# Kernel optimization log

Hardware: AMD Instinct MI355X
Metric: run time of the kernel (lower is better)

Reference implementation:

```python
import jax, jax.numpy as jnp
import numpy as np

N, E, D, H, C, ED = 50000, 800000, 128, 4, 32, 1
EFF = H * C  # 128 == D, so residual proj is Identity
FFN_H = 2 * EFF


def setup_inputs() -> dict:
    key = jax.random.key(0)
    ks = jax.random.split(key, 16)
    def p(k, shape, fan_in):
        return jax.random.normal(k, shape, dtype=jnp.float32) / np.sqrt(fan_in)
    return {
        "x": jax.random.normal(ks[0], (N, D), dtype=jnp.float32),
        "edge_attr": jax.random.normal(ks[1], (E, ED), dtype=jnp.float32),
        "W_l": p(ks[2], (D, EFF), D),
        "b_l": jnp.zeros((EFF,), jnp.float32),
        "W_r": p(ks[3], (D, EFF), D),
        "b_r": jnp.zeros((EFF,), jnp.float32),
        "W_e": p(ks[4], (ED, EFF), ED),
        "att": p(ks[5], (H, C), C),
        "bias_out": jnp.zeros((EFF,), jnp.float32),
        "W_gate": p(ks[6], (EFF, 1), EFF),
        "b_gate": jnp.zeros((1,), jnp.float32),
        "W_ffn1": p(ks[7], (EFF, FFN_H), EFF),
        "b_ffn1": jnp.zeros((FFN_H,), jnp.float32),
        "W_ffn2": p(ks[8], (FFN_H, EFF), FFN_H),
        "b_ffn2": jnp.zeros((EFF,), jnp.float32),
        "ln_gamma": jnp.ones((EFF,), jnp.float32),
        "ln_beta": jnp.zeros((EFF,), jnp.float32),
        "edge_index": jax.random.randint(ks[9], (2, E), 0, N, dtype=jnp.int32),
    }


def _gat_block(x, edge_attr, W_l, b_l, W_r, b_r, W_e, att, bias_out,
               W_gate, b_gate, W_ffn1, b_ffn1, W_ffn2, b_ffn2,
               ln_gamma, ln_beta, edge_index):
    n = x.shape[0]
    # add self loops (PyG default), edge_attr filled with mean
    loop = jnp.arange(n, dtype=edge_index.dtype)
    src = jnp.concatenate([edge_index[0], loop])
    dst = jnp.concatenate([edge_index[1], loop])
    ea = jnp.concatenate([edge_attr,
                          jnp.broadcast_to(edge_attr.mean(0, keepdims=True), (n, edge_attr.shape[1]))])
    # GATv2: separate source/target transforms + edge embedding
    xl = (x @ W_l + b_l).reshape(n, H, C)   # source features
    xr = (x @ W_r + b_r).reshape(n, H, C)   # target features
    ee = (ea @ W_e).reshape(-1, H, C)
    xj = xl[src]                             # [Et,H,C]
    m = jax.nn.leaky_relu(xj + xr[dst] + ee, negative_slope=0.2)
    logits = jnp.einsum('ehc,hc->eh', m, att)           # [Et,H]
    # segment softmax over destination nodes
    mx = jax.ops.segment_max(logits, dst, num_segments=n)
    ex = jnp.exp(logits - mx[dst])
    den = jax.ops.segment_sum(ex, dst, num_segments=n)
    alpha = ex / den[dst]
    out = jax.ops.segment_sum(xj * alpha[..., None], dst, num_segments=n)
    out = out.reshape(n, EFF) + bias_out
    # block: ELU, gated residual (proj is Identity since D==EFF), FFN, LayerNorm
    h = jax.nn.elu(out)
    gate = jax.nn.sigmoid(h @ W_gate + b_gate)
    y = gate * h + (1.0 - gate) * x
    ffn = jax.nn.relu(y @ W_ffn1 + b_ffn1) @ W_ffn2 + b_ffn2
    y = y + ffn
    mu = y.mean(-1, keepdims=True)
    var = y.var(-1, keepdims=True)
    y = (y - mu) * jax.lax.rsqrt(var + 1e-5) * ln_gamma + ln_beta
    return y  # dropout is identity in eval mode


def reference(x, edge_attr, W_l, b_l, W_r, b_r, W_e, att, bias_out,
              W_gate, b_gate, W_ffn1, b_ffn1, W_ffn2, b_ffn2,
              ln_gamma, ln_beta, edge_index):
    return _gat_block(x, edge_attr, W_l, b_l, W_r, b_r, W_e, att, bias_out,
                      W_gate, b_gate, W_ffn1, b_ffn1, W_ffn2, b_ffn2,
                      ln_gamma, ln_beta, edge_index)
```

## Files before the change

kernel.cpp:

```cpp
#include <hip/hip_runtime.h>
#include <hip/hip_bf16.h>

#define NODES 50000
#define NEDGE 800000
#define ETOT  850000

#define NRANGE 49
#define SB 256
#define ES ((ETOT + SB - 1) / SB)

#define XF_TILES 1563
#define HIST_BLKS 256
#define FUSE_GRID (2 * HIST_BLKS + (XF_TILES - HIST_BLKS))

typedef __hip_bfloat16 bf16;
typedef __attribute__((ext_vector_type(8))) short bf16x8;
typedef __attribute__((ext_vector_type(4))) float f32x4;

__device__ __forceinline__ bf16 f2bf(float v) { return __float2bfloat16(v); }
__device__ __forceinline__ float bflo(unsigned int v) { return __uint_as_float(v << 16); }
__device__ __forceinline__ float bfhi(unsigned int v) { return __uint_as_float(v & 0xffff0000u); }

__device__ __forceinline__ unsigned int pack2(float a, float b) {
    bf16 x = f2bf(a), y = f2bf(b);
    unsigned short xs = *reinterpret_cast<unsigned short*>(&x);
    unsigned short ys = *reinterpret_cast<unsigned short*>(&y);
    return ((unsigned int)ys << 16) | (unsigned int)xs;
}

__device__ __forceinline__ unsigned short bfbits(float v) {
    bf16 x = f2bf(v);
    return *reinterpret_cast<unsigned short*>(&x);
}

__device__ __forceinline__ void hilo(float v, unsigned short& h, unsigned short& l) {
    h = bfbits(v);
    float hv = __uint_as_float((unsigned int)h << 16);
    l = bfbits(v - hv);
}

__device__ __forceinline__ void split8(const float* v, bf16x8& hi, bf16x8& lo) {
    #pragma unroll
    for (int e = 0; e < 8; ++e) {
        unsigned short hb, lb;
        hilo(v[e], hb, lb);
        ((short*)&hi)[e] = (short)hb;
        ((short*)&lo)[e] = (short)lb;
    }
}

__global__ __launch_bounds__(256) void k_wx(const float* W_l, const float* W_r,
                                            const float* W1, const float* W2,
                                            bf16* wlh, bf16* wll,
                                            bf16* wrh, bf16* wrl,
                                            bf16* w1h, bf16* w1l,
                                            bf16* w2h, bf16* w2l) {
    int tid = blockIdx.x * blockDim.x + threadIdx.x;
    unsigned short h, l;
    if (tid < 32768) {
        int m = tid >> 14, t = tid & 16383;
        int c = t >> 7, k = t & 127;
        hilo((m ? W_r : W_l)[k * 128 + c], h, l);
        (m ? wrh : wlh)[t] = *(bf16*)&h;
        (m ? wrl : wll)[t] = *(bf16*)&l;
    } else if (tid < 65536) {
        int t = tid - 32768;
        int c = t >> 7, k = t & 127;
        hilo(W1[k * 256 + c], h, l);
        w1h[t] = *(bf16*)&h;
        w1l[t] = *(bf16*)&l;
    } else {
        int t = tid - 65536;
        int c = t >> 8, k = t & 255;
        hilo(W2[k * 128 + c], h, l);
        w2h[t] = *(bf16*)&h;
        w2l[t] = *(bf16*)&l;
    }
}

__global__ __launch_bounds__(256) void k_fuse(const float* edge_attr, const int* ei,
                                              float* sum_ea, int* rhist,
                                              const float* x,
                                              const bf16* wlh, const bf16* wll,
                                              const bf16* wrh, const bf16* wrl,
                                              const float* b_l, const float* b_r,
                                              bf16* xl, bf16* xr) {
    __shared__ __align__(16) float s_x[32][132];
    const int bid = blockIdx.x;
    int idx;
    bool isprep;
    if (bid < 2 * HIST_BLKS) { isprep = (bid & 1); idx = bid >> 1; }
    else { isprep = false; idx = HIST_BLKS + (bid - 2 * HIST_BLKS); }

    if (isprep) {
        int* hcnt = (int*)&s_x[0][0];
        const int t = threadIdx.x;
        if (t < 64) hcnt[t] = 0;
        __syncthreads();
        const int e0 = idx * ES;
        int e1 = e0 + ES; if (e1 > ETOT) e1 = ETOT;
        float local = 0.f;
        for (int e = e0 + t; e < e1; e += 256) {
            int dst = (e < NEDGE) ? ei[NEDGE + e] : (e - NEDGE);
            atomicAdd(&hcnt[dst >> 10], 1);
            if (e < NEDGE) local += edge_attr[e];
        }
        #pragma unroll
        for (int s = 1; s < 64; s <<= 1) local += __shfl_xor(local, s, 64);
        if ((t & 63) == 0) atomicAdd(sum_ea, local);
        __syncthreads();
        if (t < 64) rhist[idx * 64 + t] = hcnt[t];
        return;
    }

    const int tid = threadIdx.x;
    const int n0 = idx * 32;
    for (int it = 0; it < 4; ++it) {
        int idx4 = (it * 256 + tid) * 4;
        int n = idx4 >> 7, j = idx4 & 127;
        int node = n0 + n;
        float4 v = make_float4(0.f, 0.f, 0.f, 0.f);
        if (node < NODES) v = *(const float4*)(x + node * 128 + j);
        *(float4*)&s_x[n][j] = v;
    }
    __syncthreads();

    const int wv4  = tid >> 6;
    const int ln   = tid & 63;
    const int lrow = ln & 15;
    const int lk8  = (ln >> 4) << 3;
    const int m    = wv4 >> 1;
    const int cb   = (wv4 & 1) * 64;
    const bf16* Bh = m ? wrh : wlh;
    const bf16* Bl = m ? wrl : wll;
    const float* bias = m ? b_r : b_l;

    f32x4 acc[2][4];
    #pragma unroll
    for (int mt = 0; mt < 2; ++mt)
        #pragma unroll
        for (int i = 0; i < 4; ++i)
            acc[mt][i] = (f32x4){0.f, 0.f, 0.f, 0.f};
    #pragma unroll
    for (int kk = 0; kk < 4; ++kk) {
        int k0 = kk * 32 + lk8;
        float a0f[8], a1f[8];
        *(float4*)&a0f[0] = *(const float4*)&s_x[lrow][k0];
        *(float4*)&a0f[4] = *(const float4*)&s_x[lrow][k0 + 4];
        *(float4*)&a1f[0] = *(const float4*)&s_x[16 + lrow][k0];
        *(float4*)&a1f[4] = *(const float4*)&s_x[16 + lrow][k0 + 4];
        bf16x8 a0h, a0l, a1h, a1l;
        split8(a0f, a0h, a0l);
        split8(a1f, a1h, a1l);
        #pragma unroll
        for (int i = 0; i < 4; ++i) {
            int col = cb + (i << 4) + lrow;
            bf16x8 bh = *(const bf16x8*)(Bh + col * 128 + k0);
            bf16x8 bl = *(const bf16x8*)(Bl + col * 128 + k0);
            acc[0][i] = __builtin_amdgcn_mfma_f32_16x16x32_bf16(a0l, bh, acc[0][i], 0, 0, 0);
            acc[0][i] = __builtin_amdgcn_mfma_f32_16x16x32_bf16(a0h, bl, acc[0][i], 0, 0, 0);
            acc[0][i] = __builtin_amdgcn_mfma_f32_16x16x32_bf16(a0h, bh, acc[0][i], 0, 0, 0);
            acc[1][i] = __builtin_amdgcn_mfma_f32_16x16x32_bf16(a1l, bh, acc[1][i], 0, 0, 0);
            acc[1][i] = __builtin_amdgcn_mfma_f32_16x16x32_bf16(a1h, bl, acc[1][i], 0, 0, 0);
            acc[1][i] = __builtin_amdgcn_mfma_f32_16x16x32_bf16(a1h, bh, acc[1][i], 0, 0, 0);
        }
    }
    __syncthreads();
    bf16* s_o = (bf16*)&s_x[0][0];
    #pragma unroll
    for (int mt = 0; mt < 2; ++mt) {
        #pragma unroll
        for (int i = 0; i < 4; ++i) {
            int colg = cb + (i << 4) + lrow;
            float bv = bias[colg];
            #pragma unroll
            for (int r = 0; r < 4; ++r) {
                int row = (mt << 4) + ((ln >> 4) << 2) + r;
                s_o[row * 264 + m * 136 + colg] = f2bf(acc[mt][i][r] + bv);
            }
        }
    }
    __syncthreads();
    #pragma unroll
    for (int rep = 0; rep < 2; ++rep) {
        int idx2 = rep * 256 + tid;
        int row = idx2 >> 4, cc = (idx2 & 15) * 8;
        int node = n0 + row;
        if (node < NODES) {
            *(float4*)(xl + node * 128 + cc) = *(const float4*)(s_o + row * 264 + cc);
            *(float4*)(xr + node * 128 + cc) = *(const float4*)(s_o + row * 264 + 136 + cc);
        }
    }
}

__global__ __launch_bounds__(256) void k_rscan(int* rhist, int* base_r, int* off) {
    __shared__ int s_w[4];
    __shared__ int s_run;
    const int t = threadIdx.x, lane = t & 63, w = t >> 6;
    if (t == 0) s_run = 0;
    __syncthreads();
    for (int r = 0; r < NRANGE; ++r) {
        int v = rhist[t * 64 + r];
        int inc = v;
        #pragma unroll
        for (int d = 1; d < 64; d <<= 1) {
            int y = __shfl_up(inc, d, 64);
            if (lane >= d) inc += y;
        }
        if (lane == 63) s_w[w] = inc;
        __syncthreads();
        int woff = 0;
        #pragma unroll
        for (int ww = 0; ww < 4; ++ww) if (ww < w) woff += s_w[ww];
        int tot = s_w[0] + s_w[1] + s_w[2] + s_w[3];
        int runv = s_run;
        rhist[t * 64 + r] = runv + woff + (inc - v);
        if (t == 0) base_r[r] = runv;
        __syncthreads();
        if (t == 0) s_run = runv + tot;
        __syncthreads();
    }
    if (t == 0) { base_r[NRANGE] = ETOT; off[NODES] = ETOT; }
}

__global__ __launch_bounds__(256) void k_scatter(const int* ei, const float* edge_attr,
                                                 const float* sum_ea, const int* rhist,
                                                 uint2* tmp2) {
    __shared__ int cur[64];
    const int b = blockIdx.x, t = threadIdx.x;
    if (t < 64) cur[t] = rhist[b * 64 + t];
    __syncthreads();
    const float meanv = sum_ea[0] * (1.f / (float)NEDGE);
    const int e0 = b * ES;
    int e1 = e0 + ES; if (e1 > ETOT) e1 = ETOT;
    for (int e = e0 + t; e < e1; e += 256) {
        int src, dst; float eav;
        if (e < NEDGE) { src = ei[e]; dst = ei[NEDGE + e]; eav = edge_attr[e]; }
        else           { src = e - NEDGE; dst = src; eav = meanv; }
        int pos = atomicAdd(&cur[dst >> 10], 1);
        tmp2[pos] = make_uint2((unsigned int)dst,
                               ((unsigned int)bfbits(eav) << 16) | (unsigned int)src);
    }
}

__global__ __launch_bounds__(1024) void k_group(const uint2* tmp2, const int* base_r,
                                                int* off, unsigned int* perm) {
    __shared__ int lcnt[1024];
    __shared__ int s_w16[16];
    const int r = blockIdx.x, t = threadIdx.x;
    const int lane = t & 63, w = t >> 6;
    const int n0 = r << 10;
    const int s0 = base_r[r], s1 = base_r[r + 1];
    lcnt[t] = 0;
    __syncthreads();
    for (int i = s0 + t; i < s1; i += 1024) {
        int d = (int)tmp2[i].x;
        atomicAdd(&lcnt[d - n0], 1);
    }
    __syncthreads();
    int v = lcnt[t];
    int inc = v;
    #pragma unroll
    for (int d = 1; d < 64; d <<= 1) {
        int y = __shfl_up(inc, d, 64);
        if (lane >= d) inc += y;
    }
    if (lane == 63) s_w16[w] = inc;
    __syncthreads();
    int woff = 0;
    #pragma unroll
    for (int ww = 0; ww < 16; ++ww) if (ww < w) woff += s_w16[ww];
    int pos0 = s0 + woff + (inc - v);
    lcnt[t] = pos0;
    if (n0 + t < NODES) off[n0 + t] = pos0;
    __syncthreads();
    for (int i = s0 + t; i < s1; i += 1024) {
        uint2 p = tmp2[i];
        int pos = atomicAdd(&lcnt[(int)p.x - n0], 1);
        perm[pos] = p.y;
    }
}

__global__ __launch_bounds__(256) void k_agg(const unsigned int* xl32,
                                             const unsigned int* xr32,
                                             const unsigned int* perm, const int* off,
                                             const float* W_e, const float* att,
                                             float* outp) {
    const int lane = threadIdx.x & 63;
    const int wave0 = blockIdx.x * 4 + (threadIdx.x >> 6);
    const int nwaves = gridDim.x * 4;
    const int c = 2 * lane;
    const float we1 = W_e[c], we2 = W_e[c + 1];
    const float a1 = att[c], a2 = att[c + 1];
    for (int n = wave0; n < NODES; n += nwaves) {
        unsigned int xru = xr32[n * 64 + lane];
        float xr1 = bflo(xru), xr2 = bfhi(xru);
        int s0 = off[n], s1 = off[n + 1];
        float m = -1e30f, l = 0.f, acc1 = 0.f, acc2 = 0.f;
        int j = s0;
        for (; j + 4 <= s1; j += 4) {
            unsigned int u0 = perm[j];
            unsigned int u1 = perm[j + 1];
            unsigned int u2 = perm[j + 2];
            unsigned int u3 = perm[j + 3];
            unsigned int g0 = xl32[(u0 & 0xffffu) * 64 + lane];
            unsigned int g1 = xl32[(u1 & 0xffffu) * 64 + lane];
            unsigned int g2 = xl32[(u2 & 0xffffu) * 64 + lane];
            unsigned int g3 = xl32[(u3 & 0xffffu) * 64 + lane];
            float e0 = bfhi(u0), e1 = bfhi(u1), e2 = bfhi(u2), e3 = bfhi(u3);
            float x01 = bflo(g0), x02 = bfhi(g0);
            float x11 = bflo(g1), x12 = bfhi(g1);
            float x21 = bflo(g2), x22 = bfhi(g2);
            float x31 = bflo(g3), x32 = bfhi(g3);
            float p0, p1, p2, p3;
            {
                float v1 = x01 + xr1 + e0 * we1, v2 = x02 + xr2 + e0 * we2;
                v1 = (v1 > 0.f) ? v1 : 0.2f * v1;
                v2 = (v2 > 0.f) ? v2 : 0.2f * v2;
                p0 = v1 * a1 + v2 * a2;
            }
            {
                float v1 = x11 + xr1 + e1 * we1, v2 = x12 + xr2 + e1 * we2;
                v1 = (v1 > 0.f) ? v1 : 0.2f * v1;
                v2 = (v2 > 0.f) ? v2 : 0.2f * v2;
                p1 = v1 * a1 + v2 * a2;
            }
            {
                float v1 = x21 + xr1 + e2 * we1, v2 = x22 + xr2 + e2 * we2;
                v1 = (v1 > 0.f) ? v1 : 0.2f * v1;
                v2 = (v2 > 0.f) ? v2 : 0.2f * v2;
                p2 = v1 * a1 + v2 * a2;
            }
            {
                float v1 = x31 + xr1 + e3 * we1, v2 = x32 + xr2 + e3 * we2;
                v1 = (v1 > 0.f) ? v1 : 0.2f * v1;
                v2 = (v2 > 0.f) ? v2 : 0.2f * v2;
                p3 = v1 * a1 + v2 * a2;
            }
            p0 += __shfl_xor(p0, 1, 64); p1 += __shfl_xor(p1, 1, 64);
            p2 += __shfl_xor(p2, 1, 64); p3 += __shfl_xor(p3, 1, 64);
            p0 += __shfl_xor(p0, 2, 64); p1 += __shfl_xor(p1, 2, 64);
            p2 += __shfl_xor(p2, 2, 64); p3 += __shfl_xor(p3, 2, 64);
            p0 += __shfl_xor(p0, 4, 64); p1 += __shfl_xor(p1, 4, 64);
            p2 += __shfl_xor(p2, 4, 64); p3 += __shfl_xor(p3, 4, 64);
            p0 += __shfl_xor(p0, 8, 64); p1 += __shfl_xor(p1, 8, 64);
            p2 += __shfl_xor(p2, 8, 64); p3 += __shfl_xor(p3, 8, 64);
            float nm = fmaxf(fmaxf(m, fmaxf(p0, p1)), fmaxf(p2, p3));
            float sc = __expf(m - nm);
            float E0 = __expf(p0 - nm);
            float E1 = __expf(p1 - nm);
            float E2 = __expf(p2 - nm);
            float E3 = __expf(p3 - nm);
            l = l * sc + E0 + E1 + E2 + E3;
            acc1 = acc1 * sc + E0 * x01 + E1 * x11 + E2 * x21 + E3 * x31;
            acc2 = acc2 * sc + E0 * x02 + E1 * x12 + E2 * x22 + E3 * x32;
            m = nm;
        }
        for (; j < s1; ++j) {
            unsigned int u0 = perm[j];
            unsigned int g0 = xl32[(u0 & 0xffffu) * 64 + lane];
            float e0 = bfhi(u0);
            float x01 = bflo(g0), x02 = bfhi(g0);
            float v1 = x01 + xr1 + e0 * we1, v2 = x02 + xr2 + e0 * we2;
            v1 = (v1 > 0.f) ? v1 : 0.2f * v1;
            v2 = (v2 > 0.f) ? v2 : 0.2f * v2;
            float p = v1 * a1 + v2 * a2;
            p += __shfl_xor(p, 1, 64);
            p += __shfl_xor(p, 2, 64);
            p += __shfl_xor(p, 4, 64);
            p += __shfl_xor(p, 8, 64);
            float nm = fmaxf(m, p);
            float sc = __expf(m - nm);
            float ee = __expf(p - nm);
            l = l * sc + ee;
            acc1 = acc1 * sc + ee * x01;
            acc2 = acc2 * sc + ee * x02;
            m = nm;
        }
        float inv = 1.f / fmaxf(l, 1e-30f);
        *(float2*)(outp + n * 128 + c) = make_float2(acc1 * inv, acc2 * inv);
    }
}

__global__ __launch_bounds__(256) void k_epi(const float* out_agg, const float* x,
                                             const float* bias_out,
                                             const float* W_gate, const float* b_gate,
                                             const bf16* w1h, const bf16* w1l,
                                             const float* b_ffn1,
                                             const bf16* w2h, const bf16* w2l,
                                             const float* b_ffn2,
                                             const float* gamma, const float* beta,
                                             float* out) {
    __shared__ __align__(16) bf16 s_yh[32][136];
    __shared__ __align__(16) bf16 s_yl[32][136];
    __shared__ __align__(16) bf16 s_th[32][264];
    __shared__ __align__(16) bf16 s_tl[32][264];
    __shared__ float s_g[32];
    __shared__ float s_mu[32], s_rs[32];
    const int tid = threadIdx.x;
    const int n0 = blockIdx.x * 32;
    int nn = NODES - n0; if (nn > 32) nn = 32;

    for (int it = 0; it < 4; ++it) {
        int idx4 = (it * 256 + tid) * 4;
        int n = idx4 >> 7, j = idx4 & 127;
        float4 w = make_float4(0.f, 0.f, 0.f, 0.f);
        if (n < nn) {
            float4 v  = *(const float4*)(out_agg + (n0 + n) * 128 + j);
            float4 bv = *(const float4*)(bias_out + j);
            float t0 = v.x + bv.x, t1 = v.y + bv.y;
            float t2 = v.z + bv.z, t3 = v.w + bv.w;
            w.x = (t0 > 0.f) ? t0 : (__expf(t0) - 1.f);
            w.y = (t1 > 0.f) ? t1 : (__expf(t1) - 1.f);
            w.z = (t2 > 0.f) ? t2 : (__expf(t2) - 1.f);
            w.w = (t3 > 0.f) ? t3 : (__expf(t3) - 1.f);
        }
        unsigned short hx, lx, hy, ly, hz, lz, hw, lw;
        hilo(w.x, hx, lx); hilo(w.y, hy, ly);
        hilo(w.z, hz, lz); hilo(w.w, hw, lw);
        uint2 uh = make_uint2((unsigned)hx | ((unsigned)hy << 16),
                              (unsigned)hz | ((unsigned)hw << 16));
        uint2 ul = make_uint2((unsigned)lx | ((unsigned)ly << 16),
                              (unsigned)lz | ((unsigned)lw << 16));
        *(uint2*)&s_yh[n][j] = uh;
        *(uint2*)&s_yl[n][j] = ul;
    }
    __syncthreads();
    {
        int n = tid >> 3, kb = (tid & 7) * 16;
        float g = 0.f;
        #pragma unroll
        for (int k = 0; k < 16; k += 4) {
            uint2 uh = *(const uint2*)&s_yh[n][kb + k];
            uint2 ul = *(const uint2*)&s_yl[n][kb + k];
            float4 wg = *(const float4*)(W_gate + kb + k);
            g += (bflo(uh.x) + bflo(ul.x)) * wg.x;
            g += (bfhi(uh.x) + bfhi(ul.x)) * wg.y;
            g += (bflo(uh.y) + bflo(ul.y)) * wg.z;
            g += (bfhi(uh.y) + bfhi(ul.y)) * wg.w;
        }
        g += __shfl_xor(g, 1, 64);
        g += __shfl_xor(g, 2, 64);
        g += __shfl_xor(g, 4, 64);
        if ((tid & 7) == 0) s_g[n] = 1.f / (1.f + __expf(-(g + b_gate[0])));
    }
    __syncthreads();
    for (int it = 0; it < 4; ++it) {
        int idx4 = (it * 256 + tid) * 4;
        int n = idx4 >> 7, j = idx4 & 127;
        if (n < nn) {
            float g = s_g[n];
            float4 xv = *(const float4*)(x + (n0 + n) * 128 + j);
            uint2 uh = *(const uint2*)&s_yh[n][j];
            uint2 ul = *(const uint2*)&s_yl[n][j];
            float y0 = g * (bflo(uh.x) + bflo(ul.x)) + (1.f - g) * xv.x;
            float y1 = g * (bfhi(uh.x) + bfhi(ul.x)) + (1.f - g) * xv.y;
            float y2 = g * (bflo(uh.y) + bflo(ul.y)) + (1.f - g) * xv.z;
            float y3 = g * (bfhi(uh.y) + bfhi(ul.y)) + (1.f - g) * xv.w;
            unsigned short hx, lx, hy, ly, hz, lz, hw, lw;
            hilo(y0, hx, lx); hilo(y1, hy, ly);
            hilo(y2, hz, lz); hilo(y3, hw, lw);
            uint2 nh = make_uint2((unsigned)hx | ((unsigned)hy << 16),
                                  (unsigned)hz | ((unsigned)hw << 16));
            uint2 nl = make_uint2((unsigned)lx | ((unsigned)ly << 16),
                                  (unsigned)lz | ((unsigned)lw << 16));
            *(uint2*)&s_yh[n][j] = nh;
            *(uint2*)&s_yl[n][j] = nl;
        }
    }
    __syncthreads();

    const int wv   = tid >> 6;
    const int ln   = tid & 63;
    const int lrow = ln & 15;
    const int lk8  = (ln >> 4) << 3;

    f32x4 acc1[2][4];
    #pragma unroll
    for (int mt = 0; mt < 2; ++mt)
        #pragma unroll
        for (int i = 0; i < 4; ++i)
            acc1[mt][i] = (f32x4){0.f, 0.f, 0.f, 0.f};
    #pragma unroll
    for (int kk = 0; kk < 4; ++kk) {
        int k0 = kk * 32 + lk8;
        bf16x8 a0h = *(const bf16x8*)&s_yh[lrow][k0];
        bf16x8 a0l = *(const bf16x8*)&s_yl[lrow][k0];
        bf16x8 a1h = *(const bf16x8*)&s_yh[16 + lrow][k0];
        bf16x8 a1l = *(const bf16x8*)&s_yl[16 + lrow][k0];
        #pragma unroll
        for (int i = 0; i < 4; ++i) {
            int col = (wv << 6) + (i << 4) + lrow;
            bf16x8 bh = *(const bf16x8*)(w1h + col * 128 + k0);
            bf16x8 bl = *(const bf16x8*)(w1l + col * 128 + k0);
            acc1[0][i] = __builtin_amdgcn_mfma_f32_16x16x32_bf16(a0l, bh, acc1[0][i], 0, 0, 0);
            acc1[0][i] = __builtin_amdgcn_mfma_f32_16x16x32_bf16(a0h, bl, acc1[0][i], 0, 0, 0);
            acc1[0][i] = __builtin_amdgcn_mfma_f32_16x16x32_bf16(a0h, bh, acc1[0][i], 0, 0, 0);
            acc1[1][i] = __builtin_amdgcn_mfma_f32_16x16x32_bf16(a1l, bh, acc1[1][i], 0, 0, 0);
            acc1[1][i] = __builtin_amdgcn_mfma_f32_16x16x32_bf16(a1h, bl, acc1[1][i], 0, 0, 0);
            acc1[1][i] = __builtin_amdgcn_mfma_f32_16x16x32_bf16(a1h, bh, acc1[1][i], 0, 0, 0);
        }
    }
    #pragma unroll
    for (int mt = 0; mt < 2; ++mt) {
        #pragma unroll
        for (int i = 0; i < 4; ++i) {
            int col = (wv << 6) + (i << 4) + lrow;
            float bv = b_ffn1[col];
            #pragma unroll
            for (int r = 0; r < 4; ++r) {
                int row = (mt << 4) + ((ln >> 4) << 2) + r;
                float v = fmaxf(acc1[mt][i][r] + bv, 0.f);
                unsigned short h, l;
                hilo(v, h, l);
                *(unsigned short*)&s_th[row][col] = h;
                *(unsigned short*)&s_tl[row][col] = l;
            }
        }
    }
    __syncthreads();

    f32x4 acc2[2][2];
    #pragma unroll
    for (int mt = 0; mt < 2; ++mt)
        #pragma unroll
        for (int c = 0; c < 2; ++c)
            acc2[mt][c] = (f32x4){0.f, 0.f, 0.f, 0.f};
    #pragma unroll
    for (int kk = 0; kk < 8; ++kk) {
        int k0 = kk * 32 + lk8;
        bf16x8 a0h = *(const bf16x8*)&s_th[lrow][k0];
        bf16x8 a0l = *(const bf16x8*)&s_tl[lrow][k0];
        bf16x8 a1h = *(const bf16x8*)&s_th[16 + lrow][k0];
        bf16x8 a1l = *(const bf16x8*)&s_tl[16 + lrow][k0];
        #pragma unroll
        for (int c = 0; c < 2; ++c) {
            int col = (wv << 5) + (c << 4) + lrow;
            bf16x8 bh = *(const bf16x8*)(w2h + col * 256 + k0);
            bf16x8 bl = *(const bf16x8*)(w2l + col * 256 + k0);
            acc2[0][c] = __builtin_amdgcn_mfma_f32_16x16x32_bf16(a0l, bh, acc2[0][c], 0, 0, 0);
            acc2[0][c] = __builtin_amdgcn_mfma_f32_16x16x32_bf16(a0h, bl, acc2[0][c], 0, 0, 0);
            acc2[0][c] = __builtin_amdgcn_mfma_f32_16x16x32_bf16(a0h, bh, acc2[0][c], 0, 0, 0);
            acc2[1][c] = __builtin_amdgcn_mfma_f32_16x16x32_bf16(a1l, bh, acc2[1][c], 0, 0, 0);
            acc2[1][c] = __builtin_amdgcn_mfma_f32_16x16x32_bf16(a1h, bl, acc2[1][c], 0, 0, 0);
            acc2[1][c] = __builtin_amdgcn_mfma_f32_16x16x32_bf16(a1h, bh, acc2[1][c], 0, 0, 0);
        }
    }
    __syncthreads();
    float* s_z = (float*)&s_th[0][0];
    #pragma unroll
    for (int mt = 0; mt < 2; ++mt) {
        #pragma unroll
        for (int c = 0; c < 2; ++c) {
            int col = (wv << 5) + (c << 4) + lrow;
            float bv = b_ffn2[col];
            #pragma unroll
            for (int r = 0; r < 4; ++r) {
                int row = (mt << 4) + ((ln >> 4) << 2) + r;
                float yv = __bfloat162float(s_yh[row][col]) +
                           __bfloat162float(s_yl[row][col]);
                s_z[row * 132 + col] = yv + acc2[mt][c][r] + bv;
            }
        }
    }
    __syncthreads();
    {
        int n = tid >> 3, kb = (tid & 7) * 16;
        float s = 0.f, ss = 0.f;
        #pragma unroll
        for (int k = 0; k < 16; k += 4) {
            float4 v = *(const float4*)&s_z[n * 132 + kb + k];
            s  += v.x + v.y + v.z + v.w;
            ss += v.x * v.x + v.y * v.y + v.z * v.z + v.w * v.w;
        }
        s  += __shfl_xor(s, 1, 64);  ss += __shfl_xor(ss, 1, 64);
        s  += __shfl_xor(s, 2, 64);  ss += __shfl_xor(ss, 2, 64);
        s  += __shfl_xor(s, 4, 64);  ss += __shfl_xor(ss, 4, 64);
        if ((tid & 7) == 0) {
            float mu = s * (1.f / 128.f);
            float var = ss * (1.f / 128.f) - mu * mu;
            s_mu[n] = mu;
            s_rs[n] = rsqrtf(fmaxf(var, 0.f) + 1e-5f);
        }
    }
    __syncthreads();
    for (int it = 0; it < 4; ++it) {
        int idx4 = (it * 256 + tid) * 4;
        int n = idx4 >> 7, j = idx4 & 127;
        if (n < nn) {
            float mu = s_mu[n], rs = s_rs[n];
            float4 gv = *(const float4*)(gamma + j);
            float4 bv = *(const float4*)(beta + j);
            float4 v = *(const float4*)&s_z[n * 132 + j];
            float4 o;
            o.x = (v.x - mu) * rs * gv.x + bv.x;
            o.y = (v.y - mu) * rs * gv.y + bv.y;
            o.z = (v.z - mu) * rs * gv.z + bv.z;
            o.w = (v.w - mu) * rs * gv.w + bv.w;
            *(float4*)(out + (n0 + n) * 128 + j) = o;
        }
    }
}

extern "C" void kernel_launch(void* const* d_in, const int* in_sizes, int n_in,
                              void* d_out, int out_size, void* d_ws, size_t ws_size,
                              hipStream_t stream) {
    const float* x         = (const float*)d_in[0];
    const float* edge_attr = (const float*)d_in[1];
    const int* edge_index  = (const int*)d_in[17];
    float* out = (float*)d_out;

    char* base = (char*)d_ws;
    float* sum_ea  = (float*)(base + 16);
    int*   rhist   = (int*)  (base + 32);
    bf16*  w1t_hi  = (bf16*) (base + 32 + 65536);
    bf16*  w1t_lo  = (bf16*) (base + 32 + 131072);
    int*   off     = (int*)  (base + 200032);
    int*   base_r  = (int*)  (base + 400064);
    bf16*  w2t_hi  = (bf16*) (base + 400064 + 256);
    bf16*  w2t_lo  = (bf16*) (base + 400064 + 256 + 65536);
    unsigned int* perm = (unsigned int*)(base + 600064);
    bf16*  xl      = (bf16*) (base + 4000064);
    bf16*  xr      = (bf16*) (base + 16800064);
    bf16*  wxlh    = (bf16*) (base + 600064 + 1024);
    bf16*  wxll    = (bf16*) (base + 600064 + 1024 + 32768);
    bf16*  wxrh    = (bf16*) (base + 600064 + 1024 + 65536);
    bf16*  wxrl    = (bf16*) (base + 600064 + 1024 + 98304);
    uint2* tmp2    = (uint2*)d_out;

    hipMemsetAsync(sum_ea, 0, 16, stream);

    const int NTILES = (NODES + 31) / 32;

    k_wx      <<<384, 256, 0, stream>>>((const float*)d_in[2], (const float*)d_in[4],
                                        (const float*)d_in[11], (const float*)d_in[13],
                                        wxlh, wxll, wxrh, wxrl,
                                        w1t_hi, w1t_lo, w2t_hi, w2t_lo);
    k_fuse    <<<FUSE_GRID, 256, 0, stream>>>(edge_attr, edge_index, sum_ea, rhist,
                                              x, wxlh, wxll, wxrh, wxrl,
                                              (const float*)d_in[3], (const float*)d_in[5],
                                              xl, xr);
    k_rscan   <<<1, 256, 0, stream>>>(rhist, base_r, off);
    k_scatter <<<SB, 256, 0, stream>>>(edge_index, edge_attr, sum_ea, rhist, tmp2);
    k_group   <<<NRANGE, 1024, 0, stream>>>(tmp2, base_r, off, perm);
    k_agg     <<<3125, 256, 0, stream>>>((const unsigned int*)xl,
                                         (const unsigned int*)xr,
                                         perm, off,
                                         (const float*)d_in[6], (const float*)d_in[7],
                                         out);
    k_epi     <<<NTILES, 256, 0, stream>>>(out, x, (const float*)d_in[8],
                                           (const float*)d_in[9], (const float*)d_in[10],
                                           w1t_hi, w1t_lo, (const float*)d_in[12],
                                           w2t_hi, w2t_lo, (const float*)d_in[14],
                                           (const float*)d_in[15], (const float*)d_in[16],
                                           out);
}
```

Before: 350.5 us.

## Shrink epilogue tile to 16 nodes and keep fp32 intermediates in LDS

The epilogue kernel now processes 16 nodes per block instead of 32, doubling the grid. It keeps the activations and FFN hidden values in fp32 shared memory and splits them into bf16 hi/lo pairs only when loading MFMA operands, rather than storing separate hi/lo bf16 arrays. The residual add is done in place in s_y. Less LDS per block should allow higher occupancy, but each block now reloads the FFN weights for half as many rows, so weight traffic per node doubles. It also relies on a split8 helper that must already exist.

```diff
diff --git a/kernel.cpp b/kernel.cpp
--- a/kernel.cpp
+++ b/kernel.cpp
@@ -391,17 +391,15 @@
                                              const float* b_ffn2,
                                              const float* gamma, const float* beta,
                                              float* out) {
-    __shared__ __align__(16) bf16 s_yh[32][136];
-    __shared__ __align__(16) bf16 s_yl[32][136];
-    __shared__ __align__(16) bf16 s_th[32][264];
-    __shared__ __align__(16) bf16 s_tl[32][264];
-    __shared__ float s_g[32];
-    __shared__ float s_mu[32], s_rs[32];
+    __shared__ __align__(16) float s_y[16][132];
+    __shared__ __align__(16) float s_t[16][260];
+    __shared__ float s_g[16];
+    __shared__ float s_mu[16], s_rs[16];
     const int tid = threadIdx.x;
-    const int n0 = blockIdx.x * 32;
-    int nn = NODES - n0; if (nn > 32) nn = 32;
-
-    for (int it = 0; it < 4; ++it) {
+    const int n0 = blockIdx.x * 16;
+    int nn = NODES - n0; if (nn > 16) nn = 16;
+
+    for (int it = 0; it < 2; ++it) {
         int idx4 = (it * 256 + tid) * 4;
         int n = idx4 >> 7, j = idx4 & 127;
         float4 w = make_float4(0.f, 0.f, 0.f, 0.f);
@@ -415,57 +413,36 @@
             w.z = (t2 > 0.f) ? t2 : (__expf(t2) - 1.f);
             w.w = (t3 > 0.f) ? t3 : (__expf(t3) - 1.f);
         }
-        unsigned short hx, lx, hy, ly, hz, lz, hw, lw;
-        hilo(w.x, hx, lx); hilo(w.y, hy, ly);
-        hilo(w.z, hz, lz); hilo(w.w, hw, lw);
-        uint2 uh = make_uint2((unsigned)hx | ((unsigned)hy << 16),
-                              (unsigned)hz | ((unsigned)hw << 16));
-        uint2 ul = make_uint2((unsigned)lx | ((unsigned)ly << 16),
-                              (unsigned)lz | ((unsigned)lw << 16));
-        *(uint2*)&s_yh[n][j] = uh;
-        *(uint2*)&s_yl[n][j] = ul;
+        *(float4*)&s_y[n][j] = w;
     }
     __syncthreads();
     {
-        int n = tid >> 3, kb = (tid & 7) * 16;
-        float g = 0.f;
-        #pragma unroll
-        for (int k = 0; k < 16; k += 4) {
-            uint2 uh = *(const uint2*)&s_yh[n][kb + k];
-            uint2 ul = *(const uint2*)&s_yl[n][kb + k];
-            float4 wg = *(const float4*)(W_gate + kb + k);
-            g += (bflo(uh.x) + bflo(ul.x)) * wg.x;
-            g += (bfhi(uh.x) + bfhi(ul.x)) * wg.y;
-            g += (bflo(uh.y) + bflo(ul.y)) * wg.z;
-            g += (bfhi(uh.y) + bfhi(ul.y)) * wg.w;
-        }
+        int n = tid >> 4, kb = (tid & 15) * 8;
+        float4 w0 = *(const float4*)(W_gate + kb);
+        float4 w1 = *(const float4*)(W_gate + kb + 4);
+        float4 h0 = *(const float4*)&s_y[n][kb];
+        float4 h1 = *(const float4*)&s_y[n][kb + 4];
+        float g = h0.x * w0.x + h0.y * w0.y + h0.z * w0.z + h0.w * w0.w
+                + h1.x * w1.x + h1.y * w1.y + h1.z * w1.z + h1.w * w1.w;
         g += __shfl_xor(g, 1, 64);
         g += __shfl_xor(g, 2, 64);
         g += __shfl_xor(g, 4, 64);
-        if ((tid & 7) == 0) s_g[n] = 1.f / (1.f + __expf(-(g + b_gate[0])));
-    }
-    __syncthreads();
-    for (int it = 0; it < 4; ++it) {
+        g += __shfl_xor(g, 8, 64);
+        if ((tid & 15) == 0) s_g[n] = 1.f / (1.f + __expf(-(g + b_gate[0])));
+    }
+    __syncthreads();
+    for (int it = 0; it < 2; ++it) {
         int idx4 = (it * 256 + tid) * 4;
         int n = idx4 >> 7, j = idx4 & 127;
         if (n < nn) {
             float g = s_g[n];
             float4 xv = *(const float4*)(x + (n0 + n) * 128 + j);
-            uint2 uh = *(const uint2*)&s_yh[n][j];
-            uint2 ul = *(const uint2*)&s_yl[n][j];
-            float y0 = g * (bflo(uh.x) + bflo(ul.x)) + (1.f - g) * xv.x;
-            float y1 = g * (bfhi(uh.x) + bfhi(ul.x)) + (1.f - g) * xv.y;
-            float y2 = g * (bflo(uh.y) + bflo(ul.y)) + (1.f - g) * xv.z;
-            float y3 = g * (bfhi(uh.y) + bfhi(ul.y)) + (1.f - g) * xv.w;
-            unsigned short hx, lx, hy, ly, hz, lz, hw, lw;
-            hilo(y0, hx, lx); hilo(y1, hy, ly);
-            hilo(y2, hz, lz); hilo(y3, hw, lw);
-            uint2 nh = make_uint2((unsigned)hx | ((unsigned)hy << 16),
-                                  (unsigned)hz | ((unsigned)hw << 16));
-            uint2 nl = make_uint2((unsigned)lx | ((unsigned)ly << 16),
-                                  (unsigned)lz | ((unsigned)lw << 16));
-            *(uint2*)&s_yh[n][j] = nh;
-            *(uint2*)&s_yl[n][j] = nl;
+            float4 h = *(float4*)&s_y[n][j];
+            h.x = g * h.x + (1.f - g) * xv.x;
+            h.y = g * h.y + (1.f - g) * xv.y;
+            h.z = g * h.z + (1.f - g) * xv.z;
+            h.w = g * h.w + (1.f - g) * xv.w;
+            *(float4*)&s_y[n][j] = h;
         }
     }
     __syncthreads();
@@ -475,108 +452,85 @@
     const int lrow = ln & 15;
     const int lk8  = (ln >> 4) << 3;
 
-    f32x4 acc1[2][4];
-    #pragma unroll
-    for (int mt = 0; mt < 2; ++mt)
-        #pragma unroll
-        for (int i = 0; i < 4; ++i)
-            acc1[mt][i] = (f32x4){0.f, 0.f, 0.f, 0.f};
+    f32x4 acc1[4];
+    #pragma unroll
+    for (int i = 0; i < 4; ++i)
+        acc1[i] = (f32x4){0.f, 0.f, 0.f, 0.f};
     #pragma unroll
     for (int kk = 0; kk < 4; ++kk) {
         int k0 = kk * 32 + lk8;
-        bf16x8 a0h = *(const bf16x8*)&s_yh[lrow][k0];
-        bf16x8 a0l = *(const bf16x8*)&s_yl[lrow][k0];
-        bf16x8 a1h = *(const bf16x8*)&s_yh[16 + lrow][k0];
-        bf16x8 a1l = *(const bf16x8*)&s_yl[16 + lrow][k0];
+        float a0f[8];
+        *(float4*)&a0f[0] = *(const float4*)&s_y[lrow][k0];
+        *(float4*)&a0f[4] = *(const float4*)&s_y[lrow][k0 + 4];
+        bf16x8 a0h, a0l;
+        split8(a0f, a0h, a0l);
         #pragma unroll
         for (int i = 0; i < 4; ++i) {
             int col = (wv << 6) + (i << 4) + lrow;
             bf16x8 bh = *(const bf16x8*)(w1h + col * 128 + k0);
             bf16x8 bl = *(const bf16x8*)(w1l + col * 128 + k0);
-            acc1[0][i] = __builtin_amdgcn_mfma_f32_16x16x32_bf16(a0l, bh, acc1[0][i], 0, 0, 0);
-            acc1[0][i] = __builtin_amdgcn_mfma_f32_16x16x32_bf16(a0h, bl, acc1[0][i], 0, 0, 0);
-            acc1[0][i] = __builtin_amdgcn_mfma_f32_16x16x32_bf16(a0h, bh, acc1[0][i], 0, 0, 0);
-            acc1[1][i] = __builtin_amdgcn_mfma_f32_16x16x32_bf16(a1l, bh, acc1[1][i], 0, 0, 0);
-            acc1[1][i] = __builtin_amdgcn_mfma_f32_16x16x32_bf16(a1h, bl, acc1[1][i], 0, 0, 0);
-            acc1[1][i] = __builtin_amdgcn_mfma_f32_16x16x32_bf16(a1h, bh, acc1[1][i], 0, 0, 0);
-        }
-    }
-    #pragma unroll
-    for (int mt = 0; mt < 2; ++mt) {
-        #pragma unroll
-        for (int i = 0; i < 4; ++i) {
-            int col = (wv << 6) + (i << 4) + lrow;
-            float bv = b_ffn1[col];
-            #pragma unroll
-            for (int r = 0; r < 4; ++r) {
-                int row = (mt << 4) + ((ln >> 4) << 2) + r;
-                float v = fmaxf(acc1[mt][i][r] + bv, 0.f);
-                unsigned short h, l;
-                hilo(v, h, l);
-                *(unsigned short*)&s_th[row][col] = h;
-                *(unsigned short*)&s_tl[row][col] = l;
-            }
-        }
-    }
-    __syncthreads();
-
-    f32x4 acc2[2][2];
-    #pragma unroll
-    for (int mt = 0; mt < 2; ++mt)
-        #pragma unroll
-        for (int c = 0; c < 2; ++c)
-            acc2[mt][c] = (f32x4){0.f, 0.f, 0.f, 0.f};
+            acc1[i] = __builtin_amdgcn_mfma_f32_16x16x32_bf16(a0l, bh, acc1[i], 0, 0, 0);
+            acc1[i] = __builtin_amdgcn_mfma_f32_16x16x32_bf16(a0h, bl, acc1[i], 0, 0, 0);
+            acc1[i] = __builtin_amdgcn_mfma_f32_16x16x32_bf16(a0h, bh, acc1[i], 0, 0, 0);
+        }
+    }
+    #pragma unroll
+    for (int i = 0; i < 4; ++i) {
+        int col = (wv << 6) + (i << 4) + lrow;
+        float bv = b_ffn1[col];
+        #pragma unroll
+        for (int r = 0; r < 4; ++r) {
+            int row = ((ln >> 4) << 2) + r;
+            s_t[row][col] = fmaxf(acc1[i][r] + bv, 0.f);
+        }
+    }
+    __syncthreads();
+
+    f32x4 acc2[2];
+    #pragma unroll
+    for (int c = 0; c < 2; ++c)
+        acc2[c] = (f32x4){0.f, 0.f, 0.f, 0.f};
     #pragma unroll
     for (int kk = 0; kk < 8; ++kk) {
         int k0 = kk * 32 + lk8;
-        bf16x8 a0h = *(const bf16x8*)&s_th[lrow][k0];
-        bf16x8 a0l = *(const bf16x8*)&s_tl[lrow][k0];
-        bf16x8 a1h = *(const bf16x8*)&s_th[16 + lrow][k0];
-        bf16x8 a1l = *(const bf16x8*)&s_tl[16 + lrow][k0];
+        float a0f[8];
+        *(float4*)&a0f[0] = *(const float4*)&s_t[lrow][k0];
+        *(float4*)&a0f[4] = *(const float4*)&s_t[lrow][k0 + 4];
+        bf16x8 a0h, a0l;
+        split8(a0f, a0h, a0l);
         #pragma unroll
         for (int c = 0; c < 2; ++c) {
             int col = (wv << 5) + (c << 4) + lrow;
             bf16x8 bh = *(const bf16x8*)(w2h + col * 256 + k0);
             bf16x8 bl = *(const bf16x8*)(w2l + col * 256 + k0);
-            acc2[0][c] = __builtin_amdgcn_mfma_f32_16x16x32_bf16(a0l, bh, acc2[0][c], 0, 0, 0);
-            acc2[0][c] = __builtin_amdgcn_mfma_f32_16x16x32_bf16(a0h, bl, acc2[0][c], 0, 0, 0);
-            acc2[0][c] = __builtin_amdgcn_mfma_f32_16x16x32_bf16(a0h, bh, acc2[0][c], 0, 0, 0);
-            acc2[1][c] = __builtin_amdgcn_mfma_f32_16x16x32_bf16(a1l, bh, acc2[1][c], 0, 0, 0);
-            acc2[1][c] = __builtin_amdgcn_mfma_f32_16x16x32_bf16(a1h, bl, acc2[1][c], 0, 0, 0);
-            acc2[1][c] = __builtin_amdgcn_mfma_f32_16x16x32_bf16(a1h, bh, acc2[1][c], 0, 0, 0);
-        }
-    }
-    __syncthreads();
-    float* s_z = (float*)&s_th[0][0];
-    #pragma unroll
-    for (int mt = 0; mt < 2; ++mt) {
-        #pragma unroll
-        for (int c = 0; c < 2; ++c) {
-            int col = (wv << 5) + (c << 4) + lrow;
-            float bv = b_ffn2[col];
-            #pragma unroll
-            for (int r = 0; r < 4; ++r) {
-                int row = (mt << 4) + ((ln >> 4) << 2) + r;
-                float yv = __bfloat162float(s_yh[row][col]) +
-                           __bfloat162float(s_yl[row][col]);
-                s_z[row * 132 + col] = yv + acc2[mt][c][r] + bv;
-            }
+            acc2[c] = __builtin_amdgcn_mfma_f32_16x16x32_bf16(a0l, bh, acc2[c], 0, 0, 0);
+            acc2[c] = __builtin_amdgcn_mfma_f32_16x16x32_bf16(a0h, bl, acc2[c], 0, 0, 0);
+            acc2[c] = __builtin_amdgcn_mfma_f32_16x16x32_bf16(a0h, bh, acc2[c], 0, 0, 0);
+        }
+    }
+    #pragma unroll
+    for (int c = 0; c < 2; ++c) {
+        int col = (wv << 5) + (c << 4) + lrow;
+        float bv = b_ffn2[col];
+        #pragma unroll
+        for (int r = 0; r < 4; ++r) {
+            int row = ((ln >> 4) << 2) + r;
+            s_y[row][col] += acc2[c][r] + bv;
         }
     }
     __syncthreads();
     {
-        int n = tid >> 3, kb = (tid & 7) * 16;
-        float s = 0.f, ss = 0.f;
-        #pragma unroll
-        for (int k = 0; k < 16; k += 4) {
-            float4 v = *(const float4*)&s_z[n * 132 + kb + k];
-            s  += v.x + v.y + v.z + v.w;
-            ss += v.x * v.x + v.y * v.y + v.z * v.z + v.w * v.w;
-        }
+        int n = tid >> 4, kb = (tid & 15) * 8;
+        float4 v0 = *(const float4*)&s_y[n][kb];
+        float4 v1 = *(const float4*)&s_y[n][kb + 4];
+        float s  = v0.x + v0.y + v0.z + v0.w + v1.x + v1.y + v1.z + v1.w;
+        float ss = v0.x * v0.x + v0.y * v0.y + v0.z * v0.z + v0.w * v0.w
+                 + v1.x * v1.x + v1.y * v1.y + v1.z * v1.z + v1.w * v1.w;
         s  += __shfl_xor(s, 1, 64);  ss += __shfl_xor(ss, 1, 64);
         s  += __shfl_xor(s, 2, 64);  ss += __shfl_xor(ss, 2, 64);
         s  += __shfl_xor(s, 4, 64);  ss += __shfl_xor(ss, 4, 64);
-        if ((tid & 7) == 0) {
+        s  += __shfl_xor(s, 8, 64);  ss += __shfl_xor(ss, 8, 64);
+        if ((tid & 15) == 0) {
             float mu = s * (1.f / 128.f);
             float var = ss * (1.f / 128.f) - mu * mu;
             s_mu[n] = mu;
@@ -584,14 +538,14 @@
         }
     }
     __syncthreads();
-    for (int it = 0; it < 4; ++it) {
+    for (int it = 0; it < 2; ++it) {
         int idx4 = (it * 256 + tid) * 4;
         int n = idx4 >> 7, j = idx4 & 127;
         if (n < nn) {
             float mu = s_mu[n], rs = s_rs[n];
             float4 gv = *(const float4*)(gamma + j);
             float4 bv = *(const float4*)(beta + j);
-            float4 v = *(const float4*)&s_z[n * 132 + j];
+            float4 v = *(const float4*)&s_y[n][j];
             float4 o;
             o.x = (v.x - mu) * rs * gv.x + bv.x;
             o.y = (v.y - mu) * rs * gv.y + bv.y;
@@ -630,7 +584,7 @@
 
     hipMemsetAsync(sum_ea, 0, 16, stream);
 
-    const int NTILES = (NODES + 31) / 32;
+    const int EPI_TILES = (NODES + 15) / 16;
 
     k_wx      <<<384, 256, 0, stream>>>((const float*)d_in[2], (const float*)d_in[4],
                                         (const float*)d_in[11], (const float*)d_in[13],
@@ -648,10 +602,10 @@
                                          perm, off,
                                          (const float*)d_in[6], (const float*)d_in[7],
                                          out);
-    k_epi     <<<NTILES, 256, 0, stream>>>(out, x, (const float*)d_in[8],
-                                           (const float*)d_in[9], (const float*)d_in[10],
-                                           w1t_hi, w1t_lo, (const float*)d_in[12],
-                                           w2t_hi, w2t_lo, (const float*)d_in[14],
-                                           (const float*)d_in[15], (const float*)d_in[16],
-                                           out);
-}
+    k_epi     <<<EPI_TILES, 256, 0, stream>>>(out, x, (const float*)d_in[8],
+                                              (const float*)d_in[9], (const float*)d_in[10],
+                                              w1t_hi, w1t_lo, (const float*)d_in[12],
+                                              w2t_hi, w2t_lo, (const float*)d_in[14],
+                                              (const float*)d_in[15], (const float*)d_in[16],
+                                              out);
+}
```

New measurement: 381.9 us. +8.9%, slower.
